# Performance work log

Measured on AMD Instinct MI355X. Metric: run time of the kernel, lower is better.

The kernel has to match this reference:

```python
import jax, jax.numpy as jnp
import numpy as np

N, E, B = 65536, 524288, 256
FEAT, EMB, NH, NB, NC = 64, 128, 4, 2, 4
OUT = EMB // NH
SLOPE = 0.01  # LeakyReLU negative_slope used everywhere in the module


def lrelu(x):
    return jnp.where(x > 0, x, SLOPE * x)


def seg_softmax(logits, seg, nseg, mask):
    # PyG softmax(src, batch): exp(x - segment_max) / (segment_sum + 1e-16)
    z = jnp.where(mask, logits, -jnp.inf)
    m = jax.ops.segment_max(z, seg, num_segments=nseg)
    m = jnp.where(jnp.isfinite(m), m, 0.0)
    e = jnp.exp(z - m[seg])
    s = jax.ops.segment_sum(e, seg, num_segments=nseg)
    return e / (s[seg] + 1e-16)


def topk_pool(x, seg, w, min_score, nseg):
    # PyG TopKPooling with min_score: score = softmax(x.w, batch);
    # keep nodes with score > min(min_score, per-graph max - 1e-7); x_out = x*score.
    score = x @ w  # [N]
    sm = seg_softmax(score, seg, nseg, jnp.ones(score.shape, bool))
    smax = jax.ops.segment_max(sm, seg, num_segments=nseg)
    thr = jnp.minimum(smax - 1e-7, min_score)
    keep = sm > thr[seg]
    xp = jnp.where(keep[:, None], x * sm[:, None], 0.0)
    return xp, keep


def graph_conv_max(x, src, dst, emask, Wrel, Wroot, b, n):
    # PyG GraphConv(aggr='max'): out = Wrel @ max_{j in N(i)} x_j + Wroot @ x_i + b
    msg = jnp.where(emask[:, None], x[src], -jnp.inf)  # [E, d]
    agg = jax.ops.segment_max(msg, dst, num_segments=n)
    agg = jnp.where(jnp.isfinite(agg), agg, 0.0)  # nodes with no in-edges -> 0 (PyG scatter fill)
    return agg @ Wrel.T + x @ Wroot.T + b


def batchnorm(x, g, b):
    # training-mode BatchNorm1d: batch statistics, biased variance, eps=1e-5
    mu = x.mean(0)
    var = x.var(0)
    return g * (x - mu) * jax.lax.rsqrt(var + 1e-5) + b


def setup_inputs() -> dict:
    key = jax.random.key(0)
    ks = jax.random.split(key, 16)
    s_feat = np.float32(1.0 / np.sqrt(FEAT))
    s_emb = np.float32(1.0 / np.sqrt(EMB))
    return {
        "x": jax.random.normal(ks[0], (N, FEAT), jnp.float32),
        "edge_index": jax.random.randint(ks[1], (2, E), 0, N, jnp.int32),
        "batch": (jnp.arange(N, dtype=jnp.int32) // (N // B)).astype(jnp.int32),
        "W_rel0": jax.random.normal(ks[2], (EMB, FEAT), jnp.float32) * s_feat,
        "W_root0": jax.random.normal(ks[3], (EMB, FEAT), jnp.float32) * s_feat,
        "b0": jnp.zeros((EMB,), jnp.float32),
        "bn0_g": jnp.ones((EMB,), jnp.float32),
        "bn0_b": jnp.zeros((EMB,), jnp.float32),
        "blk_pool_w": jax.random.normal(ks[4], (NB, NH, EMB), jnp.float32) * s_emb,
        "blk_Wrel": jax.random.normal(ks[5], (NB, NH, OUT, EMB), jnp.float32) * s_emb,
        "blk_Wroot": jax.random.normal(ks[6], (NB, NH, OUT, EMB), jnp.float32) * s_emb,
        "blk_b": jnp.zeros((NB, NH, OUT), jnp.float32),
        "blk_bn_g": jnp.ones((NB, EMB), jnp.float32),
        "blk_bn_b": jnp.zeros((NB, EMB), jnp.float32),
        "cls_pool_w": jax.random.normal(ks[7], (NC, EMB), jnp.float32) * s_emb,
        "cls_gW1": jax.random.normal(ks[8], (NC, EMB, EMB), jnp.float32) * s_emb,
        "cls_gb1": jnp.zeros((NC, EMB), jnp.float32),
        "cls_gW2": jax.random.normal(ks[9], (NC, EMB), jnp.float32) * s_emb,
        "cls_gb2": jnp.zeros((NC,), jnp.float32),
        "cls_fW1": jax.random.normal(ks[10], (NC, EMB, EMB), jnp.float32) * s_emb,
        "cls_fb1": jnp.zeros((NC, EMB), jnp.float32),
        "cls_fW2": jax.random.normal(ks[11], (NC, EMB), jnp.float32) * s_emb,
        "cls_fb2": jnp.zeros((NC,), jnp.float32),
        "batch_size": B,
    }


def reference(x, edge_index, batch, W_rel0, W_root0, b0, bn0_g, bn0_b,
              blk_pool_w, blk_Wrel, blk_Wroot, blk_b, blk_bn_g, blk_bn_b,
              cls_pool_w, cls_gW1, cls_gb1, cls_gW2, cls_gb2,
              cls_fW1, cls_fb1, cls_fW2, cls_fb2, batch_size):
    n = x.shape[0]
    src, dst = edge_index[0], edge_index[1]
    all_e = jnp.ones(src.shape, bool)
    # conv0 -> leaky_relu -> bn0
    h = lrelu(graph_conv_max(x, src, dst, all_e, W_rel0, W_root0, b0, n))
    cur = batchnorm(h, bn0_g, bn0_b)
    # multi-head blocks: pool (min_score=0.7) -> GraphConv(max) per head, scatter
    # back to original node slots, concat heads, bn, residual 0.5*(x + 0.5*bn(new))
    for bi in range(NB):
        heads = []
        for hi in range(NH):
            xp, keep = topk_pool(cur, batch, blk_pool_w[bi, hi], 0.7, batch_size)
            emask = keep[src] & keep[dst]
            o = lrelu(graph_conv_max(xp, src, dst, emask,
                                     blk_Wrel[bi, hi], blk_Wroot[bi, hi],
                                     blk_b[bi, hi], n))
            heads.append(jnp.where(keep[:, None], o, 0.0))
        new = batchnorm(jnp.concatenate(heads, axis=-1), blk_bn_g[bi], blk_bn_b[bi])
        cur = 0.5 * (cur + 0.5 * new)
    # classification heads: pool (min_score=0.8) -> GlobalAttention -> MLP -> 1
    outs = []
    for c in range(NC):
        xp, keep = topk_pool(cur, batch, cls_pool_w[c], 0.8, batch_size)
        gate = lrelu(xp @ cls_gW1[c].T + cls_gb1[c]) @ cls_gW2[c] + cls_gb2[c]  # [N]
        a = seg_softmax(gate, batch, batch_size, keep)
        pooled = jax.ops.segment_sum(a[:, None] * xp, batch, num_segments=batch_size)  # [B, EMB]
        y = lrelu(pooled @ cls_fW1[c].T + cls_fb1[c]) @ cls_fW2[c] + cls_fb2[c]  # [B]
        outs.append(y)
    logits = jnp.stack(outs, axis=-1)  # [B, NC]
    return jax.nn.log_softmax(logits, axis=-1)
```

## Files before the change

### kernel.cpp

```cpp
#include <hip/hip_runtime.h>
#include <math.h>

#define NN 65536
#define NE 524288
#define NG 256
#define SLOPE 0.01f
#define CAP 131072

__device__ __forceinline__ float lrelu(float v){ return v > 0.f ? v : SLOPE*v; }

__device__ __forceinline__ float blockMax4(float v, float* s4){
  #pragma unroll
  for(int o=32;o>0;o>>=1) v = fmaxf(v, __shfl_down(v, o, 64));
  int t = threadIdx.x;
  __syncthreads();
  if((t&63)==0) s4[t>>6] = v;
  __syncthreads();
  return fmaxf(fmaxf(s4[0], s4[1]), fmaxf(s4[2], s4[3]));
}
__device__ __forceinline__ float blockSum4(float v, float* s4){
  #pragma unroll
  for(int o=32;o>0;o>>=1) v += __shfl_down(v, o, 64);
  int t = threadIdx.x;
  __syncthreads();
  if((t&63)==0) s4[t>>6] = v;
  __syncthreads();
  return (s4[0]+s4[1])+(s4[2]+s4[3]);
}

__global__ __launch_bounds__(256) void k_count(const int* __restrict__ ei, int* __restrict__ deg){
  int e = blockIdx.x*256 + threadIdx.x;
  if(e < NE) atomicAdd(&deg[ei[NE + e]], 1);
}

__global__ __launch_bounds__(1024) void k_scan(const int* __restrict__ deg,
      int* __restrict__ offs, int* __restrict__ cursor){
  __shared__ int part[1024];
  int t = threadIdx.x;
  const int4* d4 = (const int4*)(deg + t*64);
  int4 buf[16];
  int s=0;
  #pragma unroll
  for(int i=0;i<16;i++){ buf[i]=d4[i]; s += buf[i].x+buf[i].y+buf[i].z+buf[i].w; }
  part[t]=s;
  __syncthreads();
  for(int off=1; off<1024; off<<=1){
    int v = (t>=off)? part[t-off] : 0;
    __syncthreads();
    part[t] += v;
    __syncthreads();
  }
  int run = (t==0)? 0 : part[t-1];
  #pragma unroll
  for(int i=0;i<16;i++){
    int4 d = buf[i];
    int4 o;
    o.x = run; run += d.x;
    o.y = run; run += d.y;
    o.z = run; run += d.z;
    o.w = run; run += d.w;
    ((int4*)(offs + t*64))[i] = o;
    ((int4*)(cursor + t*64))[i] = o;
  }
  if(t==1023) offs[NN] = run;
}

__global__ __launch_bounds__(256) void k_scatter(const int* __restrict__ ei,
      int* __restrict__ cursor, int* __restrict__ csr){
  int e = blockIdx.x*256 + threadIdx.x;
  if(e < NE){
    int d = ei[NE + e];
    int p = atomicAdd(&cursor[d], 1);
    csr[p] = ei[e];
  }
}

__global__ __launch_bounds__(256) void k_agg0(const float* __restrict__ x,
    const int* __restrict__ offs, const int* __restrict__ csr, float* __restrict__ agg0){
  int tid = blockIdx.x*256 + threadIdx.x;
  int node = tid>>4, q = tid&15;
  int e0 = offs[node], e1 = offs[node+1];
  float4 acc = make_float4(0.f,0.f,0.f,0.f);
  if(e0 < e1){
    acc = make_float4(-INFINITY,-INFINITY,-INFINITY,-INFINITY);
    const int last = e1 - 1;
    for(int e=e0; e<e1; e+=8){
      int si[8];
      #pragma unroll
      for(int u=0;u<8;u++){
        int ee = e+u; ee = ee<last? ee : last;
        si[u] = csr[ee];
      }
      float4 v[8];
      #pragma unroll
      for(int u=0;u<8;u++) v[u] = ((const float4*)x)[si[u]*16 + q];
      #pragma unroll
      for(int u=0;u<8;u++){
        acc.x=fmaxf(acc.x,v[u].x); acc.y=fmaxf(acc.y,v[u].y);
        acc.z=fmaxf(acc.z,v[u].z); acc.w=fmaxf(acc.w,v[u].w);
      }
    }
  }
  ((float4*)agg0)[node*16 + q] = acc;
}

__global__ __launch_bounds__(256, 2) void k_conv0mm(
    const float* __restrict__ agg0, const float* __restrict__ x,
    const float* __restrict__ Wrel, const float* __restrict__ Wroot,
    const float* __restrict__ b0, float* __restrict__ cur,
    float* __restrict__ bnsum, float* __restrict__ bnsq){
  __shared__ float4 As[2048];
  __shared__ float4 Ws[2048];
  const int t = threadIdx.x;
  const int tn = t & 15;
  const int tc = t >> 4;
  float acc[8][8];
  #pragma unroll
  for(int i=0;i<8;i++)
    #pragma unroll
    for(int j=0;j<8;j++) acc[i][j]=0.f;

  const size_t tileoff = (size_t)blockIdx.x * 8192;
  #pragma unroll 1
  for(int ch=0; ch<2; ch++){
    const float4* gA = (const float4*)((ch==0? agg0 : x) + tileoff);
    const float4* gW = (const float4*)(ch==0? Wrel : Wroot);
    __syncthreads();
    #pragma unroll
    for(int i=0;i<8;i++){
      int idx = t + i*256;
      int n = idx>>4, k4 = idx&15;
      int sw = n*16 + ((k4 + (n>>3))&15);
      As[sw] = gA[idx];
      Ws[sw] = gW[idx];
    }
    __syncthreads();
    #pragma unroll 4
    for(int k4=0;k4<16;k4++){
      float4 a4[8], w4[8];
      #pragma unroll
      for(int i=0;i<8;i++) a4[i] = As[(tn*8+i)*16 + ((k4+tn)&15)];
      #pragma unroll
      for(int i=0;i<8;i++) w4[i] = Ws[(tc*8+i)*16 + ((k4+tc)&15)];
      #pragma unroll
      for(int i=0;i<8;i++)
        #pragma unroll
        for(int j=0;j<8;j++){
          acc[i][j] = fmaf(a4[i].x, w4[j].x, acc[i][j]);
          acc[i][j] = fmaf(a4[i].y, w4[j].y, acc[i][j]);
          acc[i][j] = fmaf(a4[i].z, w4[j].z, acc[i][j]);
          acc[i][j] = fmaf(a4[i].w, w4[j].w, acc[i][j]);
        }
    }
  }

  float bj[8];
  #pragma unroll
  for(int j=0;j<8;j++) bj[j] = b0[tc*8+j];
  float cs[8], cq[8];
  #pragma unroll
  for(int j=0;j<8;j++){ cs[j]=0.f; cq[j]=0.f; }
  const int nbase = blockIdx.x*128;
  #pragma unroll
  for(int i=0;i<8;i++){
    int node = nbase + tn*8 + i;
    float v[8];
    #pragma unroll
    for(int j=0;j<8;j++){
      v[j] = lrelu(acc[i][j] + bj[j]);
      cs[j] += v[j]; cq[j] += v[j]*v[j];
    }
    float4 o0 = make_float4(v[0],v[1],v[2],v[3]);
    float4 o1 = make_float4(v[4],v[5],v[6],v[7]);
    ((float4*)cur)[node*32 + tc*2 + 0] = o0;
    ((float4*)cur)[node*32 + tc*2 + 1] = o1;
  }
  __syncthreads();
  float* reds = (float*)As;
  float* redq = (float*)Ws;
  #pragma unroll
  for(int j=0;j<8;j++){
    reds[(tc*8+j)*16 + tn] = cs[j];
    redq[(tc*8+j)*16 + tn] = cq[j];
  }
  __syncthreads();
  if(t<128){
    float S=0.f, Q=0.f;
    #pragma unroll
    for(int i=0;i<16;i++){ S += reds[t*16+i]; Q += redq[t*16+i]; }
    atomicAdd(&bnsum[t], S);
    atomicAdd(&bnsq[t], Q);
  }
}

__global__ __launch_bounds__(256) void k_scores(const float* __restrict__ cur0,
    const float* __restrict__ bns0, const float* __restrict__ bnq0,
    const float* __restrict__ g0,
    const float* __restrict__ pw0, const float* __restrict__ pw1,
    const float* __restrict__ pwc,
    float* __restrict__ scores0, float* __restrict__ pre1, float* __restrict__ pre2){
  __shared__ __align__(16) float w[12][128];
  __shared__ float sc0s[128];
  const int t = threadIdx.x;
  if(t<128){
    float mu = bns0[t]*(1.0f/NN);
    float var = bnq0[t]*(1.0f/NN) - mu*mu;
    sc0s[t] = g0[t]*rsqrtf(var+1e-5f);
  }
  __syncthreads();
  for(int i=t;i<512;i+=256){
    int h=i>>7, j=i&127;
    float s = sc0s[j];
    w[h][j]   = pw0[i]*s;
    w[4+h][j] = pw1[i]*(0.5f*s);
    w[8+h][j] = pwc[i]*(0.25f*s);
  }
  __syncthreads();
  const int tid = blockIdx.x*256 + t;
  const int n = tid>>5, k = tid&31;
  float4 v = ((const float4*)cur0)[tid];
  float a[12];
  #pragma unroll
  for(int q=0;q<12;q++){
    float4 wv = *(const float4*)&w[q][k*4];
    a[q] = v.x*wv.x + v.y*wv.y + v.z*wv.z + v.w*wv.w;
  }
  #pragma unroll
  for(int o=16;o>0;o>>=1){
    #pragma unroll
    for(int q=0;q<12;q++) a[q] += __shfl_down(a[q], o, 32);
  }
  if(k==0){
    ((float4*)scores0)[n] = make_float4(a[0],a[1],a[2],a[3]);
    ((float4*)pre1)[n]    = make_float4(a[4],a[5],a[6],a[7]);
    ((float4*)pre2)[n]    = make_float4(a[8],a[9],a[10],a[11]);
  }
}

__global__ __launch_bounds__(256) void k_poolselW(const float* __restrict__ scores,
    float minscore, float* __restrict__ sm4, int* __restrict__ cnt,
    int* __restrict__ wl, int* __restrict__ idxP){
  const int t = threadIdx.x, g = blockIdx.x;
  const int h = t>>6, l = t&63;
  const int n0 = g*256;
  float s[4];
  #pragma unroll
  for(int i=0;i<4;i++) s[i] = scores[(size_t)(n0 + l + i*64)*4 + h];
  float m = fmaxf(fmaxf(s[0],s[1]),fmaxf(s[2],s[3]));
  #pragma unroll
  for(int o=32;o>0;o>>=1) m = fmaxf(m, __shfl_xor(m, o, 64));
  float e[4], es=0.f;
  #pragma unroll
  for(int i=0;i<4;i++){ e[i]=expf(s[i]-m); es+=e[i]; }
  #pragma unroll
  for(int o=32;o>0;o>>=1) es += __shfl_xor(es, o, 64);
  float inv = 1.f/(es+1e-16f);
  float sm[4];
  float mx = -INFINITY;
  #pragma unroll
  for(int i=0;i<4;i++){ sm[i]=e[i]*inv; mx=fmaxf(mx,sm[i]); }
  #pragma unroll
  for(int o=32;o>0;o>>=1) mx = fmaxf(mx, __shfl_xor(mx, o, 64));
  float thr = fminf(mx - 1e-7f, minscore);
  #pragma unroll
  for(int i=0;i<4;i++){
    int n = n0 + l + i*64;
    sm4[(size_t)n*4 + h] = sm[i];
    int slot = -1;
    if(sm[i] > thr){
      int p = atomicAdd(cnt, 1);
      if(p < CAP){ slot = p; wl[p] = (h<<16) | n; }
    }
    idxP[(size_t)h*NN + n] = slot;
  }
}

__global__ __launch_bounds__(256) void k_blockconv0(const float* __restrict__ cur0,
    const int* __restrict__ offs, const int* __restrict__ csr,
    const int* __restrict__ idxP, const float* __restrict__ sm4,
    const int* __restrict__ cnt, const int* __restrict__ wl,
    const float* __restrict__ Wrel, const float* __restrict__ Wroot,
    const float* __restrict__ bias,
    float* __restrict__ new1c, float* __restrict__ bnsum, float* __restrict__ bnsq,
    const float* __restrict__ bns0, const float* __restrict__ bnq0,
    const float* __restrict__ g0, const float* __restrict__ b0bn){
  __shared__ __align__(16) float aggs[8][128];
  __shared__ __align__(16) float xps[8][128];
  __shared__ __align__(16) float scv[128];
  __shared__ __align__(16) float ofv[128];
  const int t = threadIdx.x, grp = t>>5, lane = t&31;
  if(t<128){
    float mu = bns0[t]*(1.0f/NN);
    float var = bnq0[t]*(1.0f/NN) - mu*mu;
    float sv = g0[t]*rsqrtf(var+1e-5f);
    scv[t]=sv; ofv[t]=b0bn[t]-mu*sv;
  }
  __syncthreads();
  const float4 s4l = *(const float4*)&scv[lane*4];
  const float4 o4l = *(const float4*)&ofv[lane*4];
  int total = *cnt; if(total > CAP) total = CAP;
  for(int item = blockIdx.x*8 + grp; item < total; item += gridDim.x*8){
    const int wv = wl[item];
    const int h = wv>>16, n = wv & 0xFFFF;
    const size_t hn = (size_t)h*NN;
    const float smn = sm4[(size_t)n*4+h];
    const int e0 = offs[n], e1 = offs[n+1];
    float4 acc = make_float4(-INFINITY,-INFINITY,-INFINITY,-INFINITY);
    bool any = false;
    for(int e=e0;e<e1;e++){
      int s = csr[e];
      if(idxP[hn + s] >= 0){
        any = true;
        float sv = sm4[(size_t)s*4+h];
        float4 v = ((const float4*)cur0)[s*32 + lane];
        v.x = (v.x*s4l.x + o4l.x)*sv; v.y = (v.y*s4l.y + o4l.y)*sv;
        v.z = (v.z*s4l.z + o4l.z)*sv; v.w = (v.w*s4l.w + o4l.w)*sv;
        acc.x = fmaxf(acc.x, v.x); acc.y = fmaxf(acc.y, v.y);
        acc.z = fmaxf(acc.z, v.z); acc.w = fmaxf(acc.w, v.w);
      }
    }
    if(!any) acc = make_float4(0.f,0.f,0.f,0.f);
    *(float4*)&aggs[grp][lane*4] = acc;
    float4 xv = ((const float4*)cur0)[n*32 + lane];
    xv.x = (xv.x*s4l.x + o4l.x)*smn; xv.y = (xv.y*s4l.y + o4l.y)*smn;
    xv.z = (xv.z*s4l.z + o4l.z)*smn; xv.w = (xv.w*s4l.w + o4l.w)*smn;
    *(float4*)&xps[grp][lane*4] = xv;
    const float* Wr = Wrel  + (size_t)(h*32+lane)*128;
    const float* Wo = Wroot + (size_t)(h*32+lane)*128;
    float o = bias[h*32+lane];
    for(int k=0;k<32;k++){
      float4 a  = *(const float4*)&aggs[grp][k*4];
      float4 xx = *(const float4*)&xps[grp][k*4];
      float4 wr = ((const float4*)Wr)[k];
      float4 wo = ((const float4*)Wo)[k];
      o += a.x*wr.x + a.y*wr.y + a.z*wr.z + a.w*wr.w;
      o += xx.x*wo.x + xx.y*wo.y + xx.z*wo.z + xx.w*wo.w;
    }
    o = lrelu(o);
    new1c[(size_t)item*32 + lane] = o;
    atomicAdd(&bnsum[h*32+lane], o);
    atomicAdd(&bnsq[h*32+lane], o*o);
  }
}

__global__ __launch_bounds__(256) void k_poolsel1(
    const float* __restrict__ pre1, float* __restrict__ pre2,
    const int* __restrict__ cnt0, const int* __restrict__ wl0,
    const float* __restrict__ new1c,
    const float* __restrict__ bnsA, const float* __restrict__ bnqA,
    const float* __restrict__ g1v,
    const float* __restrict__ pw1, const float* __restrict__ pwc,
    float minscore, float* __restrict__ sm4out,
    int* __restrict__ cnt1, int* __restrict__ wl1, int* __restrict__ idx1P){
  __shared__ float s1s[128];
  __shared__ __align__(16) float w1s[4][128];
  __shared__ __align__(16) float wcs[4][128];
  __shared__ float patch1[256][4];
  const int t = threadIdx.x, g = blockIdx.x;
  if(t<128){
    float mu = bnsA[t]*(1.0f/NN);
    float var = bnqA[t]*(1.0f/NN) - mu*mu;
    s1s[t] = g1v[t]*rsqrtf(var+1e-5f);
  }
  for(int i=t;i<512;i+=256){ w1s[i>>7][i&127]=pw1[i]; wcs[i>>7][i&127]=pwc[i]; }
  #pragma unroll
  for(int h=0;h<4;h++) patch1[t][h]=0.f;
  __syncthreads();
  int total0 = *cnt0; if(total0 > CAP) total0 = CAP;
  for(int i=t; i<total0; i+=256){
    int wv = wl0[i];
    int n = wv & 0xFFFF, hp = wv>>16;
    if((n>>8)==g){
      int nl = n & 255;
      float d[4]={0.f,0.f,0.f,0.f}, d2[4]={0.f,0.f,0.f,0.f};
      for(int l=0;l<32;l++){
        int j = hp*32+l;
        float base = new1c[(size_t)i*32+l] * s1s[j];
        #pragma unroll
        for(int h=0;h<4;h++){ d[h]+=base*w1s[h][j]; d2[h]+=base*wcs[h][j]; }
      }
      #pragma unroll
      for(int h=0;h<4;h++){
        atomicAdd(&patch1[nl][h], 0.25f*d[h]);
        atomicAdd(&pre2[n*4+h], 0.125f*d2[h]);
      }
    }
  }
  __syncthreads();
  const int h = t>>6, l = t&63;
  const int n0 = g*256;
  float s[4];
  #pragma unroll
  for(int i=0;i<4;i++){
    int nl = l + i*64;
    s[i] = pre1[(size_t)(n0+nl)*4 + h] + patch1[nl][h];
  }
  float m = fmaxf(fmaxf(s[0],s[1]),fmaxf(s[2],s[3]));
  #pragma unroll
  for(int o=32;o>0;o>>=1) m = fmaxf(m, __shfl_xor(m, o, 64));
  float e[4], es=0.f;
  #pragma unroll
  for(int i=0;i<4;i++){ e[i]=expf(s[i]-m); es+=e[i]; }
  #pragma unroll
  for(int o=32;o>0;o>>=1) es += __shfl_xor(es, o, 64);
  float inv = 1.f/(es+1e-16f);
  float sm[4];
  float mx = -INFINITY;
  #pragma unroll
  for(int i=0;i<4;i++){ sm[i]=e[i]*inv; mx=fmaxf(mx,sm[i]); }
  #pragma unroll
  for(int o=32;o>0;o>>=1) mx = fmaxf(mx, __shfl_xor(mx, o, 64));
  float thr = fminf(mx - 1e-7f, minscore);
  #pragma unroll
  for(int i=0;i<4;i++){
    int n = n0 + l + i*64;
    sm4out[(size_t)n*4 + h] = sm[i];
    int slot = -1;
    if(sm[i] > thr){
      int p = atomicAdd(cnt1, 1);
      if(p < CAP){ slot = p; wl1[p] = (h<<16) | n; }
    }
    idx1P[(size_t)h*NN + n] = slot;
  }
}

__global__ __launch_bounds__(256) void k_blockconv1(const float* __restrict__ cur0,
    const int* __restrict__ offs, const int* __restrict__ csr,
    const int* __restrict__ idx0P, const float* __restrict__ new1c,
    const int* __restrict__ idx1P, const float* __restrict__ sm41,
    const int* __restrict__ cnt1, const int* __restrict__ wl1,
    const float* __restrict__ Wrel, const float* __restrict__ Wroot,
    const float* __restrict__ bias,
    float* __restrict__ new2c, float* __restrict__ bnsum, float* __restrict__ bnsq,
    const float* __restrict__ bns0, const float* __restrict__ bnq0,
    const float* __restrict__ g0, const float* __restrict__ b0bn,
    const float* __restrict__ bnsA, const float* __restrict__ bnqA,
    const float* __restrict__ g1v, const float* __restrict__ b1v){
  __shared__ __align__(16) float aggs[8][128];
  __shared__ __align__(16) float xps[8][128];
  __shared__ __align__(16) float sc0s[128], of0s[128], s1s[128], o1s[128];
  const int t = threadIdx.x, grp = t>>5, lane = t&31;
  if(t<128){
    float mu = bns0[t]*(1.0f/NN);
    float var = bnq0[t]*(1.0f/NN) - mu*mu;
    float sv = g0[t]*rsqrtf(var+1e-5f);
    sc0s[t]=sv; of0s[t]=b0bn[t]-mu*sv;
    float mu1 = bnsA[t]*(1.0f/NN);
    float var1 = bnqA[t]*(1.0f/NN) - mu1*mu1;
    float s1 = g1v[t]*rsqrtf(var1+1e-5f);
    s1s[t]=s1; o1s[t]=b1v[t]-mu1*s1;
  }
  __syncthreads();
  const float4 s0l = *(const float4*)&sc0s[lane*4];
  const float4 o0l = *(const float4*)&of0s[lane*4];
  const float4 s1l = *(const float4*)&s1s[lane*4];
  const float4 o1l = *(const float4*)&o1s[lane*4];
  const int hb = lane>>3;
  const size_t hbn = (size_t)hb*NN;
  int total = *cnt1; if(total > CAP) total = CAP;
  for(int item = blockIdx.x*8 + grp; item < total; item += gridDim.x*8){
    const int wv = wl1[item];
    const int h = wv>>16, n = wv & 0xFFFF;
    const size_t hn = (size_t)h*NN;
    const float smn = sm41[(size_t)n*4+h];
    const int e0 = offs[n], e1 = offs[n+1];
    float4 acc = make_float4(-INFINITY,-INFINITY,-INFINITY,-INFINITY);
    bool any = false;
    for(int e=e0;e<e1;e++){
      int s = csr[e];
      if(idx1P[hn + s] >= 0){
        any = true;
        float sv = sm41[(size_t)s*4+h];
        float4 c0 = ((const float4*)cur0)[s*32 + lane];
        float4 v;
        v.x = 0.5f*(s0l.x*c0.x+o0l.x) + 0.25f*o1l.x;
        v.y = 0.5f*(s0l.y*c0.y+o0l.y) + 0.25f*o1l.y;
        v.z = 0.5f*(s0l.z*c0.z+o0l.z) + 0.25f*o1l.z;
        v.w = 0.5f*(s0l.w*c0.w+o0l.w) + 0.25f*o1l.w;
        int i0 = idx0P[hbn + s];
        if(i0 >= 0){
          float4 nv = ((const float4*)(new1c + (size_t)i0*32))[lane&7];
          v.x += 0.25f*s1l.x*nv.x; v.y += 0.25f*s1l.y*nv.y;
          v.z += 0.25f*s1l.z*nv.z; v.w += 0.25f*s1l.w*nv.w;
        }
        v.x*=sv; v.y*=sv; v.z*=sv; v.w*=sv;
        acc.x = fmaxf(acc.x, v.x); acc.y = fmaxf(acc.y, v.y);
        acc.z = fmaxf(acc.z, v.z); acc.w = fmaxf(acc.w, v.w);
      }
    }
    if(!any) acc = make_float4(0.f,0.f,0.f,0.f);
    *(float4*)&aggs[grp][lane*4] = acc;
    {
      float4 c0 = ((const float4*)cur0)[n*32 + lane];
      float4 v;
      v.x = 0.5f*(s0l.x*c0.x+o0l.x) + 0.25f*o1l.x;
      v.y = 0.5f*(s0l.y*c0.y+o0l.y) + 0.25f*o1l.y;
      v.z = 0.5f*(s0l.z*c0.z+o0l.z) + 0.25f*o1l.z;
      v.w = 0.5f*(s0l.w*c0.w+o0l.w) + 0.25f*o1l.w;
      int i0 = idx0P[hbn + n];
      if(i0 >= 0){
        float4 nv = ((const float4*)(new1c + (size_t)i0*32))[lane&7];
        v.x += 0.25f*s1l.x*nv.x; v.y += 0.25f*s1l.y*nv.y;
        v.z += 0.25f*s1l.z*nv.z; v.w += 0.25f*s1l.w*nv.w;
      }
      v.x*=smn; v.y*=smn; v.z*=smn; v.w*=smn;
      *(float4*)&xps[grp][lane*4] = v;
    }
    const float* Wr = Wrel  + (size_t)(h*32+lane)*128;
    const float* Wo = Wroot + (size_t)(h*32+lane)*128;
    float o = bias[h*32+lane];
    for(int k=0;k<32;k++){
      float4 a  = *(const float4*)&aggs[grp][k*4];
      float4 xx = *(const float4*)&xps[grp][k*4];
      float4 wr = ((const float4*)Wr)[k];
      float4 wo = ((const float4*)Wo)[k];
      o += a.x*wr.x + a.y*wr.y + a.z*wr.z + a.w*wr.w;
      o += xx.x*wo.x + xx.y*wo.y + xx.z*wo.z + xx.w*wo.w;
    }
    o = lrelu(o);
    new2c[(size_t)item*32 + lane] = o;
    atomicAdd(&bnsum[h*32+lane], o);
    atomicAdd(&bnsq[h*32+lane], o*o);
  }
}

__global__ __launch_bounds__(256) void k_cls2(const float* __restrict__ cur0,
    const int* __restrict__ idx0P, const float* __restrict__ new1c,
    const int* __restrict__ idx1P, const float* __restrict__ new2c,
    const float* __restrict__ pre2, const int* __restrict__ cnt1,
    const int* __restrict__ wl1, const float* __restrict__ pwc,
    const float* __restrict__ bns0, const float* __restrict__ bnq0,
    const float* __restrict__ g0, const float* __restrict__ b0bn,
    const float* __restrict__ bnsA, const float* __restrict__ bnqA,
    const float* __restrict__ g1v, const float* __restrict__ b1v,
    const float* __restrict__ bnsB, const float* __restrict__ bnqB,
    const float* __restrict__ g2v, const float* __restrict__ b2v,
    const float* __restrict__ gW1, const float* __restrict__ gb1,
    const float* __restrict__ gW2, const float* __restrict__ gb2,
    const float* __restrict__ fW1, const float* __restrict__ fb1,
    const float* __restrict__ fW2, const float* __restrict__ fb2,
    float* __restrict__ yws, int* __restrict__ gcnt, float* __restrict__ out){
  __shared__ float red[4];
  __shared__ float sc0s[128], of0s[128], s1s[128], o1s[128], s2s[128], o2s[128];
  __shared__ float wc[128];
  __shared__ float patch[256];
  __shared__ int keptL[256];
  __shared__ float keptS[256];
  __shared__ float gateL[256];
  __shared__ __align__(16) float xk[128];
  __shared__ __align__(16) float pooled[128];
  __shared__ int nkept;
  const int t = threadIdx.x;
  const int g = blockIdx.x >> 2, c = blockIdx.x & 3;
  if(t<128){
    float mu = bns0[t]*(1.0f/NN);
    float var = bnq0[t]*(1.0f/NN) - mu*mu;
    float sv = g0[t]*rsqrtf(var+1e-5f);
    sc0s[t]=sv; of0s[t]=b0bn[t]-mu*sv;
    float mu1 = bnsA[t]*(1.0f/NN);
    float var1 = bnqA[t]*(1.0f/NN) - mu1*mu1;
    float s1 = g1v[t]*rsqrtf(var1+1e-5f);
    s1s[t]=s1; o1s[t]=b1v[t]-mu1*s1;
    float mu2 = bnsB[t]*(1.0f/NN);
    float var2 = bnqB[t]*(1.0f/NN) - mu2*mu2;
    float s2 = g2v[t]*rsqrtf(var2+1e-5f);
    s2s[t]=s2; o2s[t]=b2v[t]-mu2*s2;
    wc[t] = pwc[c*128+t];
  }
  patch[t]=0.f;
  __syncthreads();
  int total1 = *cnt1; if(total1 > CAP) total1 = CAP;
  for(int i=t; i<total1; i+=256){
    int wv = wl1[i];
    int n = wv & 0xFFFF, hp = wv>>16;
    if((n>>8)==g){
      float d=0.f;
      for(int l=0;l<32;l++){
        int j = hp*32+l;
        d += new2c[(size_t)i*32+l]*s2s[j]*wc[j];
      }
      atomicAdd(&patch[n&255], 0.25f*d);
    }
  }
  __syncthreads();
  const int n = g*256 + t;
  float sc = pre2[n*4 + c] + patch[t];
  float m = blockMax4(sc, red);
  float e = expf(sc-m);
  float ssum = blockSum4(e, red);
  float sm = e/(ssum+1e-16f);
  float smax = blockMax4(sm, red);
  float thr = fminf(smax - 1e-7f, 0.8f);
  if(t==0) nkept = 0;
  __syncthreads();
  if(sm > thr){
    int p = atomicAdd(&nkept,1);
    keptL[p]=t; keptS[p]=sm;
  }
  __syncthreads();
  const int K = nkept;
  for(int k=0;k<K;k++){
    int ln = keptL[k]; float sv = keptS[k];
    int nn = g*256 + ln;
    if(t<32){
      float4 c0 = ((const float4*)cur0)[nn*32 + t];
      float4 s0l = *(const float4*)&sc0s[t*4];
      float4 o0l = *(const float4*)&of0s[t*4];
      float4 s1l = *(const float4*)&s1s[t*4];
      float4 o1l = *(const float4*)&o1s[t*4];
      float4 s2l = *(const float4*)&s2s[t*4];
      float4 o2l = *(const float4*)&o2s[t*4];
      int hb = t>>3;
      float4 v1;
      v1.x = 0.5f*(s0l.x*c0.x+o0l.x) + 0.25f*o1l.x;
      v1.y = 0.5f*(s0l.y*c0.y+o0l.y) + 0.25f*o1l.y;
      v1.z = 0.5f*(s0l.z*c0.z+o0l.z) + 0.25f*o1l.z;
      v1.w = 0.5f*(s0l.w*c0.w+o0l.w) + 0.25f*o1l.w;
      int i0 = idx0P[(size_t)hb*NN + nn];
      if(i0 >= 0){
        float4 nv = ((const float4*)(new1c + (size_t)i0*32))[t&7];
        v1.x += 0.25f*s1l.x*nv.x; v1.y += 0.25f*s1l.y*nv.y;
        v1.z += 0.25f*s1l.z*nv.z; v1.w += 0.25f*s1l.w*nv.w;
      }
      float4 v2;
      v2.x = 0.5f*v1.x + 0.25f*o2l.x;
      v2.y = 0.5f*v1.y + 0.25f*o2l.y;
      v2.z = 0.5f*v1.z + 0.25f*o2l.z;
      v2.w = 0.5f*v1.w + 0.25f*o2l.w;
      int i1 = idx1P[(size_t)hb*NN + nn];
      if(i1 >= 0){
        float4 nv = ((const float4*)(new2c + (size_t)i1*32))[t&7];
        v2.x += 0.25f*s2l.x*nv.x; v2.y += 0.25f*s2l.y*nv.y;
        v2.z += 0.25f*s2l.z*nv.z; v2.w += 0.25f*s2l.w*nv.w;
      }
      v2.x*=sv; v2.y*=sv; v2.z*=sv; v2.w*=sv;
      *(float4*)&xk[t*4] = v2;
    }
    __syncthreads();
    float part = 0.f;
    if(t<128){
      const float* W = gW1 + (size_t)c*16384 + (size_t)t*128;
      float a = gb1[c*128+t];
      for(int f=0;f<32;f++){
        float4 xv = *(const float4*)&xk[f*4];
        float4 wv = ((const float4*)W)[f];
        a += xv.x*wv.x + xv.y*wv.y + xv.z*wv.z + xv.w*wv.w;
      }
      part = lrelu(a) * gW2[c*128+t];
    }
    float gs = blockSum4(part, red);
    if(t==0) gateL[k] = gs + gb2[c];
    __syncthreads();
  }
  float gv = (t<K)? gateL[t] : -INFINITY;
  float gm = blockMax4(gv, red);
  float ge = (t<K)? expf(gv-gm) : 0.f;
  float gsum = blockSum4(ge, red);
  if(t<K) gateL[t] = ge/(gsum+1e-16f);
  __syncthreads();
  if(t<128){
    int hb = t>>5, l = t&31;
    float acc = 0.f;
    for(int k=0;k<K;k++){
      int nn = g*256 + keptL[k];
      float c0 = cur0[(size_t)nn*128 + t];
      float v1 = 0.5f*(sc0s[t]*c0 + of0s[t]) + 0.25f*o1s[t];
      int i0 = idx0P[(size_t)hb*NN + nn];
      if(i0 >= 0) v1 += 0.25f*s1s[t]*new1c[(size_t)i0*32 + l];
      float v2 = 0.5f*v1 + 0.25f*o2s[t];
      int i1 = idx1P[(size_t)hb*NN + nn];
      if(i1 >= 0) v2 += 0.25f*s2s[t]*new2c[(size_t)i1*32 + l];
      acc += gateL[k]*keptS[k]*v2;
    }
    pooled[t]=acc;
  }
  __syncthreads();
  float part2=0.f;
  if(t<128){
    const float* F = fW1 + (size_t)c*16384 + (size_t)t*128;
    float a = fb1[c*128+t];
    for(int f=0;f<32;f++){
      float4 xv = *(const float4*)&pooled[f*4];
      float4 wv = ((const float4*)F)[f];
      a += xv.x*wv.x + xv.y*wv.y + xv.z*wv.z + xv.w*wv.w;
    }
    part2 = lrelu(a) * fW2[c*128+t];
  }
  float ysum = blockSum4(part2, red);
  if(t==0){
    yws[g*4+c] = ysum + fb2[c];
    __threadfence();
    int old = atomicAdd(&gcnt[g], 1);
    if(old == 3){
      __threadfence();
      volatile float* yv = yws + g*4;
      float y0=yv[0], y1=yv[1], y2=yv[2], y3=yv[3];
      float mm = fmaxf(fmaxf(y0,y1), fmaxf(y2,y3));
      float ll = logf(expf(y0-mm)+expf(y1-mm)+expf(y2-mm)+expf(y3-mm));
      out[g*4+0]=y0-mm-ll; out[g*4+1]=y1-mm-ll;
      out[g*4+2]=y2-mm-ll; out[g*4+3]=y3-mm-ll;
    }
  }
}

extern "C" void kernel_launch(void* const* d_in, const int* in_sizes, int n_in,
                              void* d_out, int out_size, void* d_ws, size_t ws_size,
                              hipStream_t stream){
  (void)in_sizes; (void)n_in; (void)out_size; (void)ws_size;
  const float* x     = (const float*)d_in[0];
  const int*   ei    = (const int*)d_in[1];
  const float* Wrel0 = (const float*)d_in[3];
  const float* Wroot0= (const float*)d_in[4];
  const float* b0    = (const float*)d_in[5];
  const float* bn0g  = (const float*)d_in[6];
  const float* bn0b  = (const float*)d_in[7];
  const float* bpw   = (const float*)d_in[8];
  const float* bWrel = (const float*)d_in[9];
  const float* bWroot= (const float*)d_in[10];
  const float* bbv   = (const float*)d_in[11];
  const float* bbng  = (const float*)d_in[12];
  const float* bbnb  = (const float*)d_in[13];
  const float* cpw   = (const float*)d_in[14];
  const float* gW1   = (const float*)d_in[15];
  const float* gb1   = (const float*)d_in[16];
  const float* gW2   = (const float*)d_in[17];
  const float* gb2   = (const float*)d_in[18];
  const float* fW1   = (const float*)d_in[19];
  const float* fb1   = (const float*)d_in[20];
  const float* fW2   = (const float*)d_in[21];
  const float* fb2   = (const float*)d_in[22];

  char* ws = (char*)d_ws;
  float* cur0  = (float*)(ws + 0);
  float* new1c = (float*)(ws + 33554432ull);
  float* new2c = (float*)(ws + 50331648ull);
  float* agg0  = new2c;
  int*   csr   = (int*)(ws + 67108864ull);
  float* scores0=(float*)(ws + 69206016ull);
  float* sm40  = scores0;
  float* pre1  = (float*)(ws + 70254592ull);
  float* sm41  = pre1;
  float* pre2  = (float*)(ws + 71303168ull);
  int*   wl0   = (int*)(ws + 72351744ull);
  int*   wl1   = (int*)(ws + 72876032ull);
  int*   offs  = (int*)(ws + 73400320ull);
  int*   cursor= (int*)(ws + 73666560ull);
  int*   idx0P = (int*)(ws + 73928704ull);
  int*   idx1P = (int*)(ws + 74977280ull);
  char*  Z     = ws + 76025856ull;
  int*   deg   = (int*)Z;
  float* bnsum0= (float*)(Z + 262144);
  float* bnsq0 = (float*)(Z + 262656);
  float* bnA   = (float*)(Z + 263168);
  float* bqA   = (float*)(Z + 263680);
  float* bnB   = (float*)(Z + 264192);
  float* bqB   = (float*)(Z + 264704);
  int*   cnt0  = (int*)(Z + 265216);
  int*   cnt1  = (int*)(Z + 265220);
  float* yws   = (float*)(Z + 266240);
  int*   gcnt  = (int*)(Z + 270336);

  hipMemsetAsync(Z, 0, 271360, stream);

  k_count  <<<2048,256,0,stream>>>(ei, deg);
  k_scan   <<<1,1024,0,stream>>>(deg, offs, cursor);
  k_scatter<<<2048,256,0,stream>>>(ei, cursor, csr);

  k_agg0    <<<4096,256,0,stream>>>(x, offs, csr, agg0);
  k_conv0mm <<<512,256,0,stream>>>(agg0, x, Wrel0, Wroot0, b0, cur0, bnsum0, bnsq0);

  k_scores<<<8192,256,0,stream>>>(cur0, bnsum0, bnsq0, bn0g,
                                  bpw, bpw + 512, cpw, scores0, pre1, pre2);

  k_poolselW<<<256,256,0,stream>>>(scores0, 0.7f, sm40, cnt0, wl0, idx0P);

  k_blockconv0<<<256,256,0,stream>>>(cur0, offs, csr, idx0P, sm40, cnt0, wl0,
                                     bWrel, bWroot, bbv, new1c, bnA, bqA,
                                     bnsum0, bnsq0, bn0g, bn0b);

  k_poolsel1<<<256,256,0,stream>>>(pre1, pre2, cnt0, wl0, new1c,
                                   bnA, bqA, bbng,
                                   bpw + 512, cpw,
                                   0.7f, sm41, cnt1, wl1, idx1P);

  k_blockconv1<<<256,256,0,stream>>>(cur0, offs, csr, idx0P, new1c,
                                     idx1P, sm41, cnt1, wl1,
                                     bWrel + 16384, bWroot + 16384, bbv + 128,
                                     new2c, bnB, bqB,
                                     bnsum0, bnsq0, bn0g, bn0b,
                                     bnA, bqA, bbng, bbnb);

  k_cls2<<<1024,256,0,stream>>>(cur0, idx0P, new1c, idx1P, new2c,
                                pre2, cnt1, wl1, cpw,
                                bnsum0, bnsq0, bn0g, bn0b,
                                bnA, bqA, bbng, bbnb,
                                bnB, bqB, bbng + 128, bbnb + 128,
                                gW1, gb1, gW2, gb2, fW1, fb1, fW2, fb2,
                                yws, gcnt, (float*)d_out);
}
```

Measured before the change: 386.0 us.

## Use bf16x3 split MFMA for first graph-conv matmul

```diff
diff --git a/kernel.cpp b/kernel.cpp
--- a/kernel.cpp
+++ b/kernel.cpp
@@ -6,8 +6,21 @@
 #define NG 256
 #define SLOPE 0.01f
 #define CAP 131072
+#define LDP 40
+
+typedef __attribute__((ext_vector_type(8))) short s8v;
+typedef __attribute__((ext_vector_type(4))) float f4v;
 
 __device__ __forceinline__ float lrelu(float v){ return v > 0.f ? v : SLOPE*v; }
+
+__device__ __forceinline__ unsigned short f2bf(float f){
+  unsigned u = __float_as_uint(f);
+  u += 0x7FFF + ((u>>16)&1);
+  return (unsigned short)(u>>16);
+}
+__device__ __forceinline__ float bf2f(unsigned short b){
+  return __uint_as_float(((unsigned)b)<<16);
+}
 
 __device__ __forceinline__ float blockMax4(float v, float* s4){
   #pragma unroll
@@ -109,87 +122,127 @@
     const float* __restrict__ Wrel, const float* __restrict__ Wroot,
     const float* __restrict__ b0, float* __restrict__ cur,
     float* __restrict__ bnsum, float* __restrict__ bnsq){
-  __shared__ float4 As[2048];
-  __shared__ float4 Ws[2048];
+  __shared__ unsigned short Ah[128*LDP], Am[128*LDP], Al[128*LDP];
+  __shared__ unsigned short Wh[128*LDP], Wm[128*LDP], Wl[128*LDP];
   const int t = threadIdx.x;
-  const int tn = t & 15;
-  const int tc = t >> 4;
-  float acc[8][8];
-  #pragma unroll
-  for(int i=0;i<8;i++)
+  const int wave = t>>6, lane = t&63, lm = lane&15, quad = lane>>4;
+  const int rowbase = (wave>>1)*64, colbase = (wave&1)*64;
+  const int nbase = blockIdx.x*128;
+
+  f4v acc[4][4];
+  #pragma unroll
+  for(int i=0;i<4;i++)
     #pragma unroll
-    for(int j=0;j<8;j++) acc[i][j]=0.f;
-
-  const size_t tileoff = (size_t)blockIdx.x * 8192;
+    for(int j=0;j<4;j++) acc[i][j] = (f4v){0.f,0.f,0.f,0.f};
+
   #pragma unroll 1
-  for(int ch=0; ch<2; ch++){
-    const float4* gA = (const float4*)((ch==0? agg0 : x) + tileoff);
-    const float4* gW = (const float4*)(ch==0? Wrel : Wroot);
+  for(int ch=0; ch<4; ch++){
+    const float* gA = (ch<2 ? agg0 : x);
+    const float* gW = (ch<2 ? Wrel : Wroot);
+    const int kq = (ch&1)*8;
     __syncthreads();
     #pragma unroll
-    for(int i=0;i<8;i++){
+    for(int i=0;i<4;i++){
       int idx = t + i*256;
-      int n = idx>>4, k4 = idx&15;
-      int sw = n*16 + ((k4 + (n>>3))&15);
-      As[sw] = gA[idx];
-      Ws[sw] = gW[idx];
+      int row = idx>>3, k4 = idx&7;
+      float4 va = ((const float4*)gA)[(size_t)(nbase+row)*16 + kq + k4];
+      float4 vw = ((const float4*)gW)[(size_t)row*16 + kq + k4];
+      unsigned long long ph=0, pm=0, pl=0, qh=0, qm=0, ql=0;
+      float fa[4] = {va.x,va.y,va.z,va.w};
+      float fw[4] = {vw.x,vw.y,vw.z,vw.w};
+      #pragma unroll
+      for(int e=0;e<4;e++){
+        unsigned short h = f2bf(fa[e]);
+        float r1 = fa[e]-bf2f(h);
+        unsigned short m = f2bf(r1);
+        unsigned short l = f2bf(r1-bf2f(m));
+        ph |= (unsigned long long)h << (e*16);
+        pm |= (unsigned long long)m << (e*16);
+        pl |= (unsigned long long)l << (e*16);
+        unsigned short h2 = f2bf(fw[e]);
+        float r1w = fw[e]-bf2f(h2);
+        unsigned short m2 = f2bf(r1w);
+        unsigned short l2 = f2bf(r1w-bf2f(m2));
+        qh |= (unsigned long long)h2 << (e*16);
+        qm |= (unsigned long long)m2 << (e*16);
+        ql |= (unsigned long long)l2 << (e*16);
+      }
+      int off = row*LDP + k4*4;
+      *(unsigned long long*)&Ah[off] = ph;
+      *(unsigned long long*)&Am[off] = pm;
+      *(unsigned long long*)&Al[off] = pl;
+      *(unsigned long long*)&Wh[off] = qh;
+      *(unsigned long long*)&Wm[off] = qm;
+      *(unsigned long long*)&Wl[off] = ql;
     }
     __syncthreads();
-    #pragma unroll 4
-    for(int k4=0;k4<16;k4++){
-      float4 a4[8], w4[8];
+    s8v ah[4], amv[4], alv[4];
+    #pragma unroll
+    for(int rt=0;rt<4;rt++){
+      int off = (rowbase + rt*16 + lm)*LDP + quad*8;
+      ah[rt]  = *(const s8v*)&Ah[off];
+      amv[rt] = *(const s8v*)&Am[off];
+      alv[rt] = *(const s8v*)&Al[off];
+    }
+    #pragma unroll
+    for(int ct=0;ct<4;ct++){
+      int off = (colbase + ct*16 + lm)*LDP + quad*8;
+      s8v bh = *(const s8v*)&Wh[off];
+      s8v bm = *(const s8v*)&Wm[off];
+      s8v bl = *(const s8v*)&Wl[off];
       #pragma unroll
-      for(int i=0;i<8;i++) a4[i] = As[(tn*8+i)*16 + ((k4+tn)&15)];
+      for(int rt=0;rt<4;rt++){
+        acc[rt][ct] = __builtin_amdgcn_mfma_f32_16x16x32_bf16(ah[rt],  bh, acc[rt][ct], 0,0,0);
+        acc[rt][ct] = __builtin_amdgcn_mfma_f32_16x16x32_bf16(ah[rt],  bm, acc[rt][ct], 0,0,0);
+        acc[rt][ct] = __builtin_amdgcn_mfma_f32_16x16x32_bf16(amv[rt], bh, acc[rt][ct], 0,0,0);
+        acc[rt][ct] = __builtin_amdgcn_mfma_f32_16x16x32_bf16(ah[rt],  bl, acc[rt][ct], 0,0,0);
+        acc[rt][ct] = __builtin_amdgcn_mfma_f32_16x16x32_bf16(alv[rt], bh, acc[rt][ct], 0,0,0);
+        acc[rt][ct] = __builtin_amdgcn_mfma_f32_16x16x32_bf16(amv[rt], bm, acc[rt][ct], 0,0,0);
+      }
+    }
+  }
+
+  float bj[4];
+  #pragma unroll
+  for(int ct=0;ct<4;ct++) bj[ct] = b0[colbase + ct*16 + lm];
+  float cs[4]={0.f,0.f,0.f,0.f}, cq[4]={0.f,0.f,0.f,0.f};
+  #pragma unroll
+  for(int rt=0;rt<4;rt++){
+    #pragma unroll
+    for(int ct=0;ct<4;ct++){
+      int col = colbase + ct*16 + lm;
       #pragma unroll
-      for(int i=0;i<8;i++) w4[i] = Ws[(tc*8+i)*16 + ((k4+tc)&15)];
-      #pragma unroll
-      for(int i=0;i<8;i++)
-        #pragma unroll
-        for(int j=0;j<8;j++){
-          acc[i][j] = fmaf(a4[i].x, w4[j].x, acc[i][j]);
-          acc[i][j] = fmaf(a4[i].y, w4[j].y, acc[i][j]);
-          acc[i][j] = fmaf(a4[i].z, w4[j].z, acc[i][j]);
-          acc[i][j] = fmaf(a4[i].w, w4[j].w, acc[i][j]);
-        }
-    }
-  }
-
-  float bj[8];
-  #pragma unroll
-  for(int j=0;j<8;j++) bj[j] = b0[tc*8+j];
-  float cs[8], cq[8];
-  #pragma unroll
-  for(int j=0;j<8;j++){ cs[j]=0.f; cq[j]=0.f; }
-  const int nbase = blockIdx.x*128;
-  #pragma unroll
-  for(int i=0;i<8;i++){
-    int node = nbase + tn*8 + i;
-    float v[8];
+      for(int r=0;r<4;r++){
+        int row = rowbase + rt*16 + quad*4 + r;
+        float v = lrelu(acc[rt][ct][r] + bj[ct]);
+        cur[(size_t)(nbase+row)*128 + col] = v;
+        cs[ct]+=v; cq[ct]+=v*v;
+      }
+    }
+  }
+  #pragma unroll
+  for(int o=16;o<64;o<<=1){
     #pragma unroll
-    for(int j=0;j<8;j++){
-      v[j] = lrelu(acc[i][j] + bj[j]);
-      cs[j] += v[j]; cq[j] += v[j]*v[j];
-    }
-    float4 o0 = make_float4(v[0],v[1],v[2],v[3]);
-    float4 o1 = make_float4(v[4],v[5],v[6],v[7]);
-    ((float4*)cur)[node*32 + tc*2 + 0] = o0;
-    ((float4*)cur)[node*32 + tc*2 + 1] = o1;
-  }
-  __syncthreads();
-  float* reds = (float*)As;
-  float* redq = (float*)Ws;
-  #pragma unroll
-  for(int j=0;j<8;j++){
-    reds[(tc*8+j)*16 + tn] = cs[j];
-    redq[(tc*8+j)*16 + tn] = cq[j];
+    for(int ct=0;ct<4;ct++){
+      cs[ct] += __shfl_xor(cs[ct], o, 64);
+      cq[ct] += __shfl_xor(cq[ct], o, 64);
+    }
+  }
+  __syncthreads();
+  float* redS = (float*)Ah;
+  float* redQ = (float*)Am;
+  if(quad==0){
+    #pragma unroll
+    for(int ct=0;ct<4;ct++){
+      int col = colbase + ct*16 + lm;
+      redS[(wave>>1)*128 + col] = cs[ct];
+      redQ[(wave>>1)*128 + col] = cq[ct];
+    }
   }
   __syncthreads();
   if(t<128){
-    float S=0.f, Q=0.f;
-    #pragma unroll
-    for(int i=0;i<16;i++){ S += reds[t*16+i]; Q += redq[t*16+i]; }
-    atomicAdd(&bnsum[t], S);
-    atomicAdd(&bnsq[t], Q);
+    atomicAdd(&bnsum[t], redS[t]+redS[128+t]);
+    atomicAdd(&bnsq[t],  redQ[t]+redQ[128+t]);
   }
 }
 
```

New measurement: 369.8 us (median of 2 runs). 1.04x faster.
